# Kernel optimization log

Hardware: AMD Instinct MI355X
Metric: run time of the kernel (lower is better)

Reference implementation:

```python
import jax, jax.numpy as jnp
import numpy as np

N, E, D_IN, D_H, D_OUT = 100000, 1600000, 128, 128, 16


def setup_inputs() -> dict:
    key = jax.random.key(0)
    k_x, k_e, k_w1, k_w2 = jax.random.split(key, 4)
    x = jax.random.normal(k_x, (N, D_IN), dtype=jnp.float32)
    edge_index = jax.random.randint(k_e, (2, E), 0, N, dtype=jnp.int64)
    # glorot-ish init for the two GCNConv weight matrices
    W1 = jax.random.normal(k_w1, (D_IN, D_H), dtype=jnp.float32) * (1.0 / np.sqrt(D_IN))
    b1 = jnp.zeros((D_H,), dtype=jnp.float32)
    W2 = jax.random.normal(k_w2, (D_H, D_OUT), dtype=jnp.float32) * (1.0 / np.sqrt(D_H))
    b2 = jnp.zeros((D_OUT,), dtype=jnp.float32)
    return {"x": x, "edge_index": edge_index, "W1": W1, "b1": b1, "W2": W2, "b2": b2}


def _gcn_conv(x, src, dst, norm, W, b, n):
    # linear transform, gather from source nodes, normalize, scatter-add to targets
    h = x @ W                                   # [N, d_out]
    msg = h[src] * norm[:, None]                # [E+N, d_out]
    return jax.ops.segment_sum(msg, dst, num_segments=n) + b


def reference(x, edge_index, W1, b1, W2, b2):
    n = x.shape[0]
    # GCNConv default: add self-loops, symmetric normalization D^-1/2 A D^-1/2
    loops = jnp.arange(n, dtype=edge_index.dtype)
    src = jnp.concatenate([edge_index[0], loops])
    dst = jnp.concatenate([edge_index[1], loops])
    deg = jax.ops.segment_sum(jnp.ones_like(dst, dtype=x.dtype), dst, num_segments=n)
    dinv = jnp.where(deg > 0, jax.lax.rsqrt(deg), 0.0)
    norm = dinv[src] * dinv[dst]                # [E+N]

    h = _gcn_conv(x, src, dst, norm, W1, b1, n)
    h = jax.nn.relu(h)
    # dropout is identity in eval mode (reference uses eval / deterministic path)
    out = _gcn_conv(h, src, dst, norm, W2, b2, n)
    return out
```

## Files before the change

kernel.cpp:

```cpp
#include <hip/hip_runtime.h>

typedef unsigned int uint;
typedef __attribute__((ext_vector_type(8))) short bf16x8;
typedef __attribute__((ext_vector_type(4))) float f32x4;

#define D_IN 128
#define D_H  128
#define D_OUT 16
#define NPC 512
#define NPCSH 9
#define CLDS 224
#define P1 256
#define XL_STRIDE 68
#define WT_STRIDE 68

static __device__ __forceinline__ float bflo(uint u) { return __uint_as_float(u << 16); }
static __device__ __forceinline__ float bfhi(uint u) { return __uint_as_float(u & 0xFFFF0000u); }
static __device__ __forceinline__ uint f2bf(float f) {
    uint b = __float_as_uint(f);
    return (b + 0x7FFFu + ((b >> 16) & 1u)) >> 16;
}
static __device__ __forceinline__ uint pk(float a, float b) {
    return f2bf(a) | (f2bf(b) << 16);
}


__global__ __launch_bounds__(256) void k_p1hist(const int* __restrict__ dst, int E, int N, int C,
                                                int chunk, int* __restrict__ hist1,
                                                const float* __restrict__ W1,
                                                uint* __restrict__ W1p) {
    __shared__ int h[CLDS];
    int t = threadIdx.x, b = blockIdx.x;
    if (b >= P1) {
        int p = (b - P1) * 256 + t;
        int k2 = p >> 7, f = p & 127;
        float w0 = W1[(size_t)(2 * k2) * 128 + f];
        float w1 = W1[(size_t)(2 * k2 + 1) * 128 + f];
        W1p[p] = pk(w0, w1);
        return;
    }
    for (int i = t; i < C; i += 256) h[i] = 0;
    __syncthreads();
    int e0 = b * chunk, e1 = min(e0 + chunk, E);
    for (int e = e0 + t; e < e1; e += 256) {
        int d = dst[e];
        d = max(0, min(d, N - 1));
        atomicAdd(&h[d >> NPCSH], 1);
    }
    __syncthreads();
    for (int i = t; i < C; i += 256) hist1[(size_t)i * P1 + b] = h[i];
}

__global__ __launch_bounds__(1024) void k_p1scan(int* __restrict__ hist1, int C,
                                                 int* __restrict__ cbase) {
    __shared__ int col[CLDS];
    __shared__ int sdata[1024];
    int t = threadIdx.x;
    int w = t >> 6, lane = t & 63;
    for (int i = w; i < C; i += 16) {
        int4 v = ((const int4*)hist1)[i * 64 + lane];
        int s = v.x + v.y + v.z + v.w;
        int inc = s;
        for (int off = 1; off < 64; off <<= 1) {
            int o = __shfl_up(inc, off);
            if (lane >= off) inc += o;
        }
        int excl = inc - s;
        int4 p;
        p.x = excl;
        p.y = excl + v.x;
        p.z = excl + v.x + v.y;
        p.w = excl + v.x + v.y + v.z;
        ((int4*)hist1)[i * 64 + lane] = p;
        if (lane == 63) col[i] = inc;
    }
    __syncthreads();
    int v = (t < C) ? col[t] : 0;
    sdata[t] = v;
    __syncthreads();
    for (int off = 1; off < 1024; off <<= 1) {
        int x = (t >= off) ? sdata[t - off] : 0;
        __syncthreads();
        sdata[t] += x;
        __syncthreads();
    }
    int pos = sdata[t] - v;
    if (t < C) cbase[t] = pos;
    if (t == 1023) cbase[C] = sdata[1023];
    if (t < C) col[t] = pos;
    __syncthreads();
    for (int i = w; i < C; i += 16) {
        int base = col[i];
        int4 p = ((int4*)hist1)[i * 64 + lane];
        p.x += base; p.y += base; p.z += base; p.w += base;
        ((int4*)hist1)[i * 64 + lane] = p;
    }
}

__global__ __launch_bounds__(256) void k_p1fill(const int* __restrict__ src,
                                                const int* __restrict__ dst, int E, int N, int C,
                                                int chunk, const int* __restrict__ hist1,
                                                uint* __restrict__ binned1) {
    __shared__ int cur[CLDS];
    int t = threadIdx.x, b = blockIdx.x;
    for (int i = t; i < C; i += 256) cur[i] = hist1[(size_t)i * P1 + b];
    __syncthreads();
    int e0 = b * chunk, e1 = min(e0 + chunk, E);
    for (int e = e0 + t; e < e1; e += 256) {
        int d = dst[e];
        d = max(0, min(d, N - 1));
        int s = src[e];
        s = max(0, min(s, N - 1));
        int p = atomicAdd(&cur[d >> NPCSH], 1);
        binned1[p] = ((uint)(d & (NPC - 1)) << 17) | (uint)s;
    }
}


__global__ __launch_bounds__(256) void k_p2gemm1(const uint* __restrict__ binned1,
                                                 const int* __restrict__ cbase, int N, int C,
                                                 int* __restrict__ ssrc, int* __restrict__ rowptr,
                                                 int* __restrict__ deg, float* __restrict__ dinv,
                                                 const uint* __restrict__ W1p,
                                                 const float* __restrict__ x,
                                                 uint* __restrict__ hs_b, int ntiles) {
    __shared__ uint smem[128 * WT_STRIDE + 64 * XL_STRIDE];
    int t = threadIdx.x;
    if ((int)blockIdx.x < C) {
        int* ncnt = (int*)smem;
        int* nbase_ = ncnt + NPC;
        int* sdata = nbase_ + NPC;
        int c = blockIdx.x;
        int start = cbase[c], end = cbase[c + 1];
        for (int i = t; i < NPC; i += 256) ncnt[i] = 0;
        __syncthreads();
        for (int j = start + t; j < end; j += 256) atomicAdd(&ncnt[binned1[j] >> 17], 1);
        __syncthreads();
        int v0 = ncnt[2 * t], v1 = ncnt[2 * t + 1];
        int s = v0 + v1;
        sdata[t] = s;
        __syncthreads();
        for (int off = 1; off < 256; off <<= 1) {
            int xv = (t >= off) ? sdata[t - off] : 0;
            __syncthreads();
            sdata[t] += xv;
            __syncthreads();
        }
        int pre = sdata[t] - s;
        nbase_[2 * t] = start + pre;
        nbase_[2 * t + 1] = start + pre + v0;
        __syncthreads();
        for (int i = t; i < NPC; i += 256) {
            int node = c * NPC + i;
            if (node < N) {
                deg[node] = ncnt[i];
                rowptr[node] = nbase_[i];
                dinv[node] = rsqrtf((float)ncnt[i] + 1.0f);
            }
        }
        __syncthreads();
        for (int i = t; i < NPC; i += 256) ncnt[i] = nbase_[i];
        __syncthreads();
        for (int j = start + t; j < end; j += 256) {
            uint pe = binned1[j];
            int p = atomicAdd(&ncnt[pe >> 17], 1);
            ssrc[p] = (int)(pe & 0x1FFFFu);
        }
        return;
    }
    uint* Wt = smem;
    uint* xl = smem + 128 * WT_STRIDE;
    int role = blockIdx.x - C;
    int nroles = gridDim.x - C;
    for (int p = t; p < 64 * 128; p += 256) {
        int k2 = p >> 7, f = p & 127;
        Wt[f * WT_STRIDE + k2] = W1p[p];
    }
    int w = t >> 6, lane = t & 63;
    int q = lane >> 4, m = lane & 15;
    const float4* x4 = (const float4*)x;
    for (int tile = role; tile < ntiles; tile += nroles) {
        int row0 = tile * 64;
        __syncthreads();
        for (int p = t; p < 64 * 32; p += 256) {
            int r = p >> 5, c2 = p & 31;
            int gr = row0 + r;
            float4 v = (gr < N) ? x4[(size_t)gr * 32 + c2] : make_float4(0.f, 0.f, 0.f, 0.f);
            *(uint2*)&xl[r * XL_STRIDE + 2 * c2] = make_uint2(pk(v.x, v.y), pk(v.z, v.w));
        }
        __syncthreads();
        bf16x8 afr[4][4];
#pragma unroll
        for (int rt = 0; rt < 4; rt++)
#pragma unroll
            for (int kc = 0; kc < 4; kc++)
                afr[rt][kc] = *(const bf16x8*)&xl[(rt * 16 + m) * XL_STRIDE + kc * 16 + q * 4];
        f32x4 acc[2][4];
#pragma unroll
        for (int c = 0; c < 2; c++)
#pragma unroll
            for (int rt = 0; rt < 4; rt++) acc[c][rt] = (f32x4){0.f, 0.f, 0.f, 0.f};
#pragma unroll
        for (int c = 0; c < 2; c++) {
            int f = w * 32 + c * 16 + m;
#pragma unroll
            for (int kc = 0; kc < 4; kc++) {
                bf16x8 bfr = *(const bf16x8*)&Wt[f * WT_STRIDE + kc * 16 + q * 4];
#pragma unroll
                for (int rt = 0; rt < 4; rt++)
                    acc[c][rt] = __builtin_amdgcn_mfma_f32_16x16x32_bf16(afr[rt][kc], bfr,
                                                                         acc[c][rt], 0, 0, 0);
            }
        }
        __syncthreads();
        uint* outl = xl;
#pragma unroll
        for (int rt = 0; rt < 4; rt++) {
#pragma unroll
            for (int c = 0; c < 2; c++) {
                f32x4 a = acc[c][rt];
#pragma unroll
                for (int r = 0; r < 4; r++) {
                    float v = a[r];
                    float vn = __shfl_xor(v, 1);
                    if (!(lane & 1)) {
                        int row = rt * 16 + q * 4 + r;
                        int cp = (w * 32 + c * 16 + m) >> 1;
                        outl[row * 65 + cp] = pk(v, vn);
                    }
                }
            }
        }
        __syncthreads();
        for (int p = t; p < 64 * 64; p += 256) {
            int r = p >> 6, cc = p & 63;
            int gr = row0 + r;
            if (gr < N)
                hs_b[(size_t)(cc >> 5) * N * 32 + (size_t)gr * 32 + (cc & 31)] =
                    outl[r * 65 + cc];
        }
    }
}


__global__ __launch_bounds__(256) void k_agg1(const uint* __restrict__ hs_b,
                                              const int* __restrict__ rowptr,
                                              const int* __restrict__ deg,
                                              const int* __restrict__ ssrc,
                                              const float* __restrict__ dinv,
                                              const float2* __restrict__ b1, int N,
                                              uint* __restrict__ rh_b) {
    int t = threadIdx.x;
    int w = t >> 6, lane = t & 63;
    int B = blockIdx.x;
    int xcd = B & 7;
    int half = xcd >> 2;
    int slot = xcd & 3;
    int g = B >> 3;
    int d = g * 32 + slot * 8 + w * 2 + (lane >> 5);
    bool act = (d < N);
    int dd = act ? d : 0;
    int start = rowptr[dd];
    int cnt = act ? deg[dd] : 0;
    int fl = lane & 31;
    const uint* hsH = hs_b + (size_t)half * N * 32;
    float scd = dinv[dd];
    uint sv = hsH[(size_t)dd * 32 + fl];
    float a0 = bflo(sv) * scd, a1 = bfhi(sv) * scd;
    int cnt_o = __shfl(cnt, lane ^ 32);
    int cmax = max(cnt, cnt_o);
    int base = 0;
    while (base < cmax) {
        int nb = min(cmax - base, 32);
        int nbh = min(max(cnt - base, 0), 32);
        int idxv = (fl < nbh) ? ssrc[start + base + fl] : 0;
        float dvv = dinv[idxv];
        int j = 0;
        for (; j + 16 <= nb; j += 16) {
            uint u[16];
            float dv[16];
#pragma unroll
            for (int q = 0; q < 16; q++) {
                int sj = (lane & 32) | (j + q);
                int i = __shfl(idxv, sj);
                float dq = __shfl(dvv, sj);
                dv[q] = (j + q < nbh) ? dq : 0.f;
                u[q] = hsH[(size_t)i * 32 + fl];
            }
#pragma unroll
            for (int q = 0; q < 16; q++) {
                a0 = fmaf(bflo(u[q]), dv[q], a0);
                a1 = fmaf(bfhi(u[q]), dv[q], a1);
            }
        }
        for (; j + 4 <= nb; j += 4) {
            uint u[4];
            float dv[4];
#pragma unroll
            for (int q = 0; q < 4; q++) {
                int sj = (lane & 32) | (j + q);
                int i = __shfl(idxv, sj);
                float dq = __shfl(dvv, sj);
                dv[q] = (j + q < nbh) ? dq : 0.f;
                u[q] = hsH[(size_t)i * 32 + fl];
            }
#pragma unroll
            for (int q = 0; q < 4; q++) {
                a0 = fmaf(bflo(u[q]), dv[q], a0);
                a1 = fmaf(bfhi(u[q]), dv[q], a1);
            }
        }
        for (; j < nb; j++) {
            int sj = (lane & 32) | j;
            int i = __shfl(idxv, sj);
            float dq = __shfl(dvv, sj);
            float dv = (j < nbh) ? dq : 0.f;
            uint u = hsH[(size_t)i * 32 + fl];
            a0 = fmaf(bflo(u), dv, a0);
            a1 = fmaf(bfhi(u), dv, a1);
        }
        base += nb;
    }
    if (act) {
        float2 bb = b1[half * 32 + fl];
        rh_b[(size_t)dd * 64 + half * 32 + fl] =
            pk(fmaxf(fmaf(a0, scd, bb.x), 0.f), fmaxf(fmaf(a1, scd, bb.y), 0.f));
    }
}


__global__ __launch_bounds__(256) void k_gemm2(const uint* __restrict__ rh_b,
                                               const float* __restrict__ W2,
                                               const float* __restrict__ dinv, int N,
                                               uint* __restrict__ h2_b) {
    __shared__ float Wl[D_H * D_OUT];
    int t = threadIdx.x;
    for (int i = t; i < D_H * D_OUT; i += 256) Wl[i] = W2[i];
    __syncthreads();
    int r = blockIdx.x * 256 + t;
    if (r >= N) return;
    const uint* xrow = rh_b + (size_t)r * 64;
    float acc[16];
#pragma unroll
    for (int f = 0; f < 16; f++) acc[f] = 0.f;
    for (int c = 0; c < 16; c++) {
        uint4 xv = *(const uint4*)(xrow + c * 4);
        uint xs[4] = {xv.x, xv.y, xv.z, xv.w};
#pragma unroll
        for (int u = 0; u < 4; u++) {
            int k = c * 8 + u * 2;
            float x0 = bflo(xs[u]), x1 = bfhi(xs[u]);
            const float* w0 = &Wl[k * 16];
            const float* w1 = &Wl[(k + 1) * 16];
#pragma unroll
            for (int f = 0; f < 16; f++) acc[f] = fmaf(x0, w0[f], acc[f]);
#pragma unroll
            for (int f = 0; f < 16; f++) acc[f] = fmaf(x1, w1[f], acc[f]);
        }
    }
    float sc = dinv[r];
    uint o[8];
#pragma unroll
    for (int q = 0; q < 8; q++) o[q] = pk(acc[2 * q] * sc, acc[2 * q + 1] * sc);
    *(uint4*)&h2_b[(size_t)r * 8] = make_uint4(o[0], o[1], o[2], o[3]);
    *(uint4*)&h2_b[(size_t)r * 8 + 4] = make_uint4(o[4], o[5], o[6], o[7]);
}


__global__ __launch_bounds__(256) void k_agg2(const uint* __restrict__ h2_b,
                                              const int* __restrict__ rowptr,
                                              const int* __restrict__ deg,
                                              const int* __restrict__ ssrc,
                                              const float* __restrict__ dinv,
                                              const float* __restrict__ b2, int N,
                                              float2* __restrict__ out) {
    int w = threadIdx.x >> 6, lane = threadIdx.x & 63;
    int d = blockIdx.x * 4 + w;
    if (d >= N) return;
    int slot = lane >> 3, jp = lane & 7;
    int start = rowptr[d], cnt = deg[d];
    float a0 = 0.f, a1 = 0.f;
    if (slot == 0) {
        uint sv = h2_b[(size_t)d * 8 + jp];
        a0 = bflo(sv);
        a1 = bfhi(sv);
    }
    int base = 0;
    while (base < cnt) {
        int nb = min(cnt - base, 64);
        int idxv = (lane < nb) ? ssrc[start + base + lane] : 0;
        int ng = (nb + 7) >> 3;
        if (ng <= 4) {
            int i0 = __shfl(idxv, slot);
            int i1 = __shfl(idxv, 8 + slot);
            int i2 = __shfl(idxv, 16 + slot);
            int i3 = __shfl(idxv, 24 + slot);
            uint u0 = (slot < nb) ? h2_b[(size_t)i0 * 8 + jp] : 0u;
            uint u1 = (8 + slot < nb) ? h2_b[(size_t)i1 * 8 + jp] : 0u;
            uint u2 = (16 + slot < nb) ? h2_b[(size_t)i2 * 8 + jp] : 0u;
            uint u3 = (24 + slot < nb) ? h2_b[(size_t)i3 * 8 + jp] : 0u;
            a0 += bflo(u0) + bflo(u1) + bflo(u2) + bflo(u3);
            a1 += bfhi(u0) + bfhi(u1) + bfhi(u2) + bfhi(u3);
        } else {
            for (int g = 0; g < ng; g++) {
                int j = g * 8 + slot;
                int i = __shfl(idxv, j);
                if (j < nb) {
                    uint hv = h2_b[(size_t)i * 8 + jp];
                    a0 += bflo(hv);
                    a1 += bfhi(hv);
                }
            }
        }
        base += nb;
    }
    a0 += __shfl_xor(a0, 8);
    a1 += __shfl_xor(a1, 8);
    a0 += __shfl_xor(a0, 16);
    a1 += __shfl_xor(a1, 16);
    a0 += __shfl_xor(a0, 32);
    a1 += __shfl_xor(a1, 32);
    if (slot == 0) {
        float di = dinv[d];
        out[(size_t)d * 8 + jp] =
            make_float2(fmaf(a0, di, b2[2 * jp]), fmaf(a1, di, b2[2 * jp + 1]));
    }
}


extern "C" void kernel_launch(void* const* d_in, const int* in_sizes, int n_in,
                              void* d_out, int out_size, void* d_ws, size_t ws_size,
                              hipStream_t stream) {
    const float* x  = (const float*)d_in[0];
    const int*   ei = (const int*)d_in[1];
    const float* W1 = (const float*)d_in[2];
    const float* b1 = (const float*)d_in[3];
    const float* W2 = (const float*)d_in[4];
    const float* b2 = (const float*)d_in[5];
    int N = in_sizes[0] / D_IN;
    int E = in_sizes[1] / 2;
    const int* src = ei;
    const int* dst = ei + E;
    int C = (N + NPC - 1) / NPC;
    int chunk = (E + P1 - 1) / P1;
    int ntiles = (N + 63) / 64;

    char* ws = (char*)d_ws;
    size_t off = 0;
    auto alloc = [&](size_t bytes) -> char* {
        char* p = ws + off;
        off = (off + bytes + 255) & ~(size_t)255;
        return p;
    };
    int*   hist1   = (int*)alloc((size_t)P1 * C * 4);
    int*   cbase   = (int*)alloc((size_t)(C + 1) * 4);
    uint*  binned1 = (uint*)alloc((size_t)E * 4);
    int*   ssrc    = (int*)alloc((size_t)E * 4);
    int*   rowptr  = (int*)alloc((size_t)N * 4);
    int*   deg     = (int*)alloc((size_t)N * 4);
    float* dinv    = (float*)alloc((size_t)N * 4);
    uint*  W1p     = (uint*)alloc((size_t)64 * 128 * 4);
    uint*  hs_b    = (uint*)alloc((size_t)N * 64 * 4);
    uint*  rh_b    = (uint*)alloc((size_t)N * 64 * 4);
    uint*  h2_b    = hs_b;

    k_p1hist<<<P1 + 32, 256, 0, stream>>>(dst, E, N, C, chunk, hist1, W1, W1p);
    k_p1scan<<<1, 1024, 0, stream>>>(hist1, C, cbase);
    k_p1fill<<<P1, 256, 0, stream>>>(src, dst, E, N, C, chunk, hist1, binned1);
    int g1 = min(768, ntiles);
    k_p2gemm1<<<C + g1, 256, 0, stream>>>(binned1, cbase, N, C, ssrc, rowptr, deg, dinv,
                                          W1p, x, hs_b, ntiles);
    int groups = (N + 31) / 32;
    k_agg1<<<groups * 8, 256, 0, stream>>>(hs_b, rowptr, deg, ssrc, dinv,
                                           (const float2*)b1, N, rh_b);
    k_gemm2<<<(N + 255) / 256, 256, 0, stream>>>(rh_b, W2, dinv, N, h2_b);
    k_agg2<<<(N + 3) / 4, 256, 0, stream>>>(h2_b, rowptr, deg, ssrc, dinv, b2, N,
                                            (float2*)d_out);
}
```

Measured before the change: 272.0 us.

## Fuse histogram, scan and fill into one cooperative kernel with grid syncs

Replaces the three binning kernels (histogram, single-block scan, fill) with one cooperative kernel that uses grid-wide syncs between phases. The scan is split so each of the C blocks scans its own column, then block 0 scans the column totals, and finally offsets are added back. The fill phase reuses the shared histogram array as the cursor. This removes two kernel launch gaps and the serial 1024-thread scan, at the cost of four grid barriers and cooperative launch overhead.

```diff
diff --git a/kernel.cpp b/kernel.cpp
--- a/kernel.cpp
+++ b/kernel.cpp
@@ -1,4 +1,7 @@
 #include <hip/hip_runtime.h>
+#include <hip/hip_cooperative_groups.h>
+
+namespace cg = cooperative_groups;
 
 typedef unsigned int uint;
 typedef __attribute__((ext_vector_type(8))) short bf16x8;
@@ -25,19 +28,23 @@
 }
 
 
-__global__ __launch_bounds__(256) void k_p1hist(const int* __restrict__ dst, int E, int N, int C,
-                                                int chunk, int* __restrict__ hist1,
-                                                const float* __restrict__ W1,
-                                                uint* __restrict__ W1p) {
+__global__ __launch_bounds__(256) void k_bin(const int* __restrict__ src,
+                                             const int* __restrict__ dst, int E, int N, int C,
+                                             int chunk, int* __restrict__ hist1,
+                                             uint* __restrict__ binned1,
+                                             const float* __restrict__ W1,
+                                             uint* __restrict__ W1p,
+                                             int* __restrict__ colg, int* __restrict__ cbase) {
+    cg::grid_group grid = cg::this_grid();
     __shared__ int h[CLDS];
+    __shared__ int sdata[256];
     int t = threadIdx.x, b = blockIdx.x;
-    if (b >= P1) {
-        int p = (b - P1) * 256 + t;
+    if (b < 32) {
+        int p = b * 256 + t;
         int k2 = p >> 7, f = p & 127;
         float w0 = W1[(size_t)(2 * k2) * 128 + f];
         float w1 = W1[(size_t)(2 * k2 + 1) * 128 + f];
         W1p[p] = pk(w0, w1);
-        return;
     }
     for (int i = t; i < C; i += 256) h[i] = 0;
     __syncthreads();
@@ -49,69 +56,49 @@
     }
     __syncthreads();
     for (int i = t; i < C; i += 256) hist1[(size_t)i * P1 + b] = h[i];
-}
-
-__global__ __launch_bounds__(1024) void k_p1scan(int* __restrict__ hist1, int C,
-                                                 int* __restrict__ cbase) {
-    __shared__ int col[CLDS];
-    __shared__ int sdata[1024];
-    int t = threadIdx.x;
-    int w = t >> 6, lane = t & 63;
-    for (int i = w; i < C; i += 16) {
-        int4 v = ((const int4*)hist1)[i * 64 + lane];
-        int s = v.x + v.y + v.z + v.w;
-        int inc = s;
-        for (int off = 1; off < 64; off <<= 1) {
-            int o = __shfl_up(inc, off);
-            if (lane >= off) inc += o;
-        }
-        int excl = inc - s;
-        int4 p;
-        p.x = excl;
-        p.y = excl + v.x;
-        p.z = excl + v.x + v.y;
-        p.w = excl + v.x + v.y + v.z;
-        ((int4*)hist1)[i * 64 + lane] = p;
-        if (lane == 63) col[i] = inc;
-    }
+    grid.sync();
+    if (b < C) {
+        int v = hist1[(size_t)b * P1 + t];
+        sdata[t] = v;
+        __syncthreads();
+        for (int off = 1; off < 256; off <<= 1) {
+            int x = (t >= off) ? sdata[t - off] : 0;
+            __syncthreads();
+            sdata[t] += x;
+            __syncthreads();
+        }
+        hist1[(size_t)b * P1 + t] = sdata[t] - v;
+        if (t == 255) colg[b] = sdata[255];
+    }
+    grid.sync();
+    if (b == 0) {
+        int v = (t < C) ? colg[t] : 0;
+        sdata[t] = v;
+        __syncthreads();
+        for (int off = 1; off < 256; off <<= 1) {
+            int x = (t >= off) ? sdata[t - off] : 0;
+            __syncthreads();
+            sdata[t] += x;
+            __syncthreads();
+        }
+        int pos = sdata[t] - v;
+        if (t < C) {
+            cbase[t] = pos;
+            colg[t] = pos;
+        }
+        if (t == 255) cbase[C] = sdata[255];
+    }
+    grid.sync();
+    if (b < C) hist1[(size_t)b * P1 + t] += colg[b];
+    grid.sync();
+    for (int i = t; i < C; i += 256) h[i] = hist1[(size_t)i * P1 + b];
     __syncthreads();
-    int v = (t < C) ? col[t] : 0;
-    sdata[t] = v;
-    __syncthreads();
-    for (int off = 1; off < 1024; off <<= 1) {
-        int x = (t >= off) ? sdata[t - off] : 0;
-        __syncthreads();
-        sdata[t] += x;
-        __syncthreads();
-    }
-    int pos = sdata[t] - v;
-    if (t < C) cbase[t] = pos;
-    if (t == 1023) cbase[C] = sdata[1023];
-    if (t < C) col[t] = pos;
-    __syncthreads();
-    for (int i = w; i < C; i += 16) {
-        int base = col[i];
-        int4 p = ((int4*)hist1)[i * 64 + lane];
-        p.x += base; p.y += base; p.z += base; p.w += base;
-        ((int4*)hist1)[i * 64 + lane] = p;
-    }
-}
-
-__global__ __launch_bounds__(256) void k_p1fill(const int* __restrict__ src,
-                                                const int* __restrict__ dst, int E, int N, int C,
-                                                int chunk, const int* __restrict__ hist1,
-                                                uint* __restrict__ binned1) {
-    __shared__ int cur[CLDS];
-    int t = threadIdx.x, b = blockIdx.x;
-    for (int i = t; i < C; i += 256) cur[i] = hist1[(size_t)i * P1 + b];
-    __syncthreads();
-    int e0 = b * chunk, e1 = min(e0 + chunk, E);
     for (int e = e0 + t; e < e1; e += 256) {
         int d = dst[e];
         d = max(0, min(d, N - 1));
         int s = src[e];
         s = max(0, min(s, N - 1));
-        int p = atomicAdd(&cur[d >> NPCSH], 1);
+        int p = atomicAdd(&h[d >> NPCSH], 1);
         binned1[p] = ((uint)(d & (NPC - 1)) << 17) | (uint)s;
     }
 }
@@ -454,6 +441,7 @@
     };
     int*   hist1   = (int*)alloc((size_t)P1 * C * 4);
     int*   cbase   = (int*)alloc((size_t)(C + 1) * 4);
+    int*   colg    = (int*)alloc((size_t)CLDS * 4);
     uint*  binned1 = (uint*)alloc((size_t)E * 4);
     int*   ssrc    = (int*)alloc((size_t)E * 4);
     int*   rowptr  = (int*)alloc((size_t)N * 4);
@@ -464,9 +452,11 @@
     uint*  rh_b    = (uint*)alloc((size_t)N * 64 * 4);
     uint*  h2_b    = hs_b;
 
-    k_p1hist<<<P1 + 32, 256, 0, stream>>>(dst, E, N, C, chunk, hist1, W1, W1p);
-    k_p1scan<<<1, 1024, 0, stream>>>(hist1, C, cbase);
-    k_p1fill<<<P1, 256, 0, stream>>>(src, dst, E, N, C, chunk, hist1, binned1);
+    void* bin_args[] = {(void*)&src, (void*)&dst, (void*)&E, (void*)&N, (void*)&C,
+                        (void*)&chunk, (void*)&hist1, (void*)&binned1, (void*)&W1,
+                        (void*)&W1p, (void*)&colg, (void*)&cbase};
+    hipLaunchCooperativeKernel((void*)k_bin, dim3(P1), dim3(256), bin_args, 0, stream);
+
     int g1 = min(768, ntiles);
     k_p2gemm1<<<C + g1, 256, 0, stream>>>(binned1, cbase, N, C, ssrc, rowptr, deg, dinv,
                                           W1p, x, hs_b, ntiles);
```

Result: slower. 391.5 us (+43.9%).

## Fuse histogram scan into fill kernel, each block computing its own prefix redundantly

Applied to the files above, without the earlier changes.

Removes the single-block k_p1scan launch. Each fill block now scans the whole column histogram itself, picks out its own per-bucket prefix offset and the global bucket base, then fills. Block 0 writes cbase. This trades one serial single-block kernel and the hist1 writeback for redundant scan work in all 256 blocks (C×256 ints read per block). C is about 196 here, so that redundancy stays small.

```diff
diff --git a/kernel.cpp b/kernel.cpp
--- a/kernel.cpp
+++ b/kernel.cpp
@@ -51,13 +51,18 @@
     for (int i = t; i < C; i += 256) hist1[(size_t)i * P1 + b] = h[i];
 }
 
-__global__ __launch_bounds__(1024) void k_p1scan(int* __restrict__ hist1, int C,
-                                                 int* __restrict__ cbase) {
-    __shared__ int col[CLDS];
-    __shared__ int sdata[1024];
-    int t = threadIdx.x;
+
+__global__ __launch_bounds__(256) void k_p1fill(const int* __restrict__ src,
+                                                const int* __restrict__ dst, int E, int N, int C,
+                                                int chunk, const int* __restrict__ hist1,
+                                                uint* __restrict__ binned1,
+                                                int* __restrict__ cbase) {
+    __shared__ int cur[CLDS];
+    __shared__ int tot[CLDS];
+    __shared__ int sdata[256];
+    int t = threadIdx.x, b = blockIdx.x;
     int w = t >> 6, lane = t & 63;
-    for (int i = w; i < C; i += 16) {
+    for (int i = w; i < C; i += 4) {
         int4 v = ((const int4*)hist1)[i * 64 + lane];
         int s = v.x + v.y + v.z + v.w;
         int inc = s;
@@ -66,44 +71,36 @@
             if (lane >= off) inc += o;
         }
         int excl = inc - s;
-        int4 p;
-        p.x = excl;
-        p.y = excl + v.x;
-        p.z = excl + v.x + v.y;
-        p.w = excl + v.x + v.y + v.z;
-        ((int4*)hist1)[i * 64 + lane] = p;
-        if (lane == 63) col[i] = inc;
-    }
-    __syncthreads();
-    int v = (t < C) ? col[t] : 0;
-    sdata[t] = v;
-    __syncthreads();
-    for (int off = 1; off < 1024; off <<= 1) {
+        int e = b & 3;
+        int sel = (e == 0) ? excl
+                : (e == 1) ? (excl + v.x)
+                : (e == 2) ? (excl + v.x + v.y)
+                           : (excl + v.x + v.y + v.z);
+        int pre_b = __shfl(sel, b >> 2);
+        int total = __shfl(inc, 63);
+        if (lane == 0) {
+            cur[i] = pre_b;
+            tot[i] = total;
+        }
+    }
+    __syncthreads();
+    int vv = (t < C) ? tot[t] : 0;
+    sdata[t] = vv;
+    __syncthreads();
+    for (int off = 1; off < 256; off <<= 1) {
         int x = (t >= off) ? sdata[t - off] : 0;
         __syncthreads();
         sdata[t] += x;
         __syncthreads();
     }
-    int pos = sdata[t] - v;
-    if (t < C) cbase[t] = pos;
-    if (t == 1023) cbase[C] = sdata[1023];
-    if (t < C) col[t] = pos;
-    __syncthreads();
-    for (int i = w; i < C; i += 16) {
-        int base = col[i];
-        int4 p = ((int4*)hist1)[i * 64 + lane];
-        p.x += base; p.y += base; p.z += base; p.w += base;
-        ((int4*)hist1)[i * 64 + lane] = p;
-    }
-}
-
-__global__ __launch_bounds__(256) void k_p1fill(const int* __restrict__ src,
-                                                const int* __restrict__ dst, int E, int N, int C,
-                                                int chunk, const int* __restrict__ hist1,
-                                                uint* __restrict__ binned1) {
-    __shared__ int cur[CLDS];
-    int t = threadIdx.x, b = blockIdx.x;
-    for (int i = t; i < C; i += 256) cur[i] = hist1[(size_t)i * P1 + b];
+    int pos = sdata[t] - vv;
+    if (b == 0) {
+        if (t < C) cbase[t] = pos;
+        if (t == 255) cbase[C] = sdata[255];
+    }
+    if (t < C) tot[t] = pos;
+    __syncthreads();
+    for (int i = t; i < C; i += 256) cur[i] += tot[i];
     __syncthreads();
     int e0 = b * chunk, e1 = min(e0 + chunk, E);
     for (int e = e0 + t; e < e1; e += 256) {
@@ -465,8 +462,7 @@
     uint*  h2_b    = hs_b;
 
     k_p1hist<<<P1 + 32, 256, 0, stream>>>(dst, E, N, C, chunk, hist1, W1, W1p);
-    k_p1scan<<<1, 1024, 0, stream>>>(hist1, C, cbase);
-    k_p1fill<<<P1, 256, 0, stream>>>(src, dst, E, N, C, chunk, hist1, binned1);
+    k_p1fill<<<P1, 256, 0, stream>>>(src, dst, E, N, C, chunk, hist1, binned1, cbase);
     int g1 = min(768, ntiles);
     k_p2gemm1<<<C + g1, 256, 0, stream>>>(binned1, cbase, N, C, ssrc, rowptr, deg, dinv,
                                           W1p, x, hs_b, ntiles);
```

After: 282.5 us. 3.9% more time.
